# Optimization experiments

Measured on AMD Instinct MI355X. Metric: run time of the kernel, lower is better.

The kernel has to match this reference:

```python
import math
import jax, jax.numpy as jnp
import numpy as np
from jax import lax

B, H, W = 8, 96, 96
FC, R, P, KS, TOPK = 768, 12, 16, 13, 24
SUP_TH, SUP_MIX, OPEN_K, DIL, NMS = 0.28, 0.8, 3, 3, 3

# prototype anchor metadata (buffers, deterministic)
ORI = jnp.asarray(np.linspace(0.0, math.pi, P + 1)[:-1], jnp.float32)
_lenL = np.array([0.4, 0.7, 1.0, 1.25], np.float32)
_widL = np.array([0.12, 0.18, 0.24, 0.3], np.float32)
LEN = jnp.asarray(_lenL[np.arange(P) % 4])
WID = jnp.asarray(_widL[(np.arange(P) // 4) % 4])
_ax = np.linspace(-1.0, 1.0, KS).astype(np.float32)
_gy, _gx = np.meshgrid(_ax, _ax, indexing='ij')
GX, GY = jnp.asarray(_gx), jnp.asarray(_gy)


def conv2d(x, w, b, pad=0):
    y = lax.conv_general_dilated(x, w, (1, 1), [(pad, pad), (pad, pad)],
                                 dimension_numbers=('NCHW', 'OIHW', 'NCHW'))
    return y + b[None, :, None, None]


def maxpool(x, k):
    p = k // 2
    return lax.reduce_window(x, -jnp.inf, lax.max, (1, 1, k, k), (1, 1, 1, 1),
                             [(0, 0), (0, 0), (p, p), (p, p)])


def avgpool3(x):
    s = lax.reduce_window(x, 0.0, lax.add, (1, 1, 3, 3), (1, 1, 1, 1),
                          [(0, 0), (0, 0), (1, 1), (1, 1)])
    return s / 9.0  # torch count_include_pad=True


def normalize_map(t):
    mn = t.min(axis=(-2, -1), keepdims=True)
    mx = t.max(axis=(-2, -1), keepdims=True)
    return (t - mn) / jnp.maximum(mx - mn, 1e-6)


def binary_open(m, k):
    er = 1.0 - maxpool(1.0 - m, k)
    return jnp.clip(maxpool(er, k), 0.0, 1.0)


def support_mask_fn(carrier_hp, density):
    cs = normalize_map(avgpool3(jnp.abs(carrier_hp)))
    ds = normalize_map(density)
    ev = SUP_MIX * cs + (1.0 - SUP_MIX) * ds
    m = (ev >= SUP_TH).astype(carrier_hp.dtype)
    m = binary_open(m, OPEN_K)
    m = maxpool(m, DIL)
    return jnp.clip(m, 0.0, 1.0)


def setup_inputs() -> dict:
    key = jax.random.key(0)
    ks = jax.random.split(key, 16)
    d = {
        'features': jax.random.normal(ks[0], (B, FC, H, W), jnp.float32),
        'carrier_hp': jax.random.normal(ks[1], (B, 1, H, W), jnp.float32),
        'density': jax.random.uniform(ks[2], (B, 1, H, W), jnp.float32),
        # feature_project: 1x1 conv FC->R, 3x3 conv R->R
        'w1': jax.random.normal(ks[3], (R, FC, 1, 1), jnp.float32) * (1.0 / math.sqrt(FC)),
        'b1': jnp.zeros((R,), jnp.float32),
        'w2': jax.random.normal(ks[4], (R, R, 3, 3), jnp.float32) * (1.0 / math.sqrt(R * 9)),
        'b2': jnp.zeros((R,), jnp.float32),
        # post_mix: 1x1 conv (R+4)->R, 1x1 conv R->FC
        'w3': jax.random.normal(ks[5], (R, R + 4, 1, 1), jnp.float32) * (1.0 / math.sqrt(R + 4)),
        'b3': jnp.zeros((R,), jnp.float32),
        'w4': jax.random.normal(ks[6], (FC, R, 1, 1), jnp.float32) * (1.0 / math.sqrt(R)),
        'b4': jnp.zeros((FC,), jnp.float32),
        'proto': jax.random.normal(ks[7], (P, R), jnp.float32) * 0.02,
    }
    return d


def reference(features, carrier_hp, density, w1, b1, w2, b2, w3, b3, w4, b4, proto):
    gelu = lambda x: jax.nn.gelu(x, approximate=False)
    # 1) feature projection
    proj = gelu(conv2d(gelu(conv2d(features, w1, b1, 0)), w2, b2, 1))  # [B,R,H,W]
    # 2) occupancy + support
    occ = normalize_map(jnp.abs(proj).mean(axis=1, keepdims=True))      # [B,1,H,W]
    sup = support_mask_fn(carrier_hp, density)                          # [B,1,H,W]
    # 3) NMS + top-k anchors
    scores = occ * sup
    local_max = maxpool(scores, NMS)
    peak = ((scores >= local_max) & (scores > 0.05)).astype(scores.dtype)
    flat = (scores * peak).reshape(B, -1)
    vals, idx = lax.top_k(flat, TOPK)                                   # [B,K]
    anchor_map = jnp.zeros_like(flat).at[jnp.arange(B)[:, None], idx].set(vals)
    anchor_map = anchor_map.reshape(B, 1, H, W)
    ys, xs = idx // W, idx % W
    # 4) per-anchor prototype selection
    proj_flat = proj.reshape(B, R, H * W)
    feat_at = jnp.take_along_axis(proj_flat, jnp.broadcast_to(idx[:, None, :], (B, R, TOPK)), axis=2)  # [B,R,K]
    logits = jnp.einsum('brk,pr->bkp', feat_at, proto)
    pidx = jnp.argmax(logits, axis=-1)                                  # [B,K]
    ori, ln, wd = ORI[pidx], LEN[pidx], WID[pidx]
    # 5) oriented Gaussian footprints [B,K,KS,KS]
    c = jnp.cos(ori)[..., None, None]
    s = jnp.sin(ori)[..., None, None]
    xr = c * GX + s * GY
    yr = -s * GX + c * GY
    foot = jnp.exp(-(xr / ln[..., None, None]) ** 2 - (yr / wd[..., None, None]) ** 2)
    foot = foot * vals[..., None, None]
    emb = proto[pidx]                                                   # [B,K,R]
    contrib = emb[:, :, :, None, None] * foot[:, :, None]               # [B,K,R,KS,KS]
    # 6) scatter-stamp onto canvas
    off = jnp.arange(KS) - KS // 2
    yy = ys[:, :, None, None] + off[None, None, :, None]                # [B,K,KS,KS]
    xx = xs[:, :, None, None] + off[None, None, None, :]
    valid = ((yy >= 0) & (yy < H) & (xx >= 0) & (xx < W)).astype(contrib.dtype)
    yyc = jnp.clip(yy, 0, H - 1)
    xxc = jnp.clip(xx, 0, W - 1)

    def stamp(ctr, y2, x2, v):
        c0 = jnp.zeros((R, H, W), ctr.dtype)
        return c0.at[:, y2, x2].add(jnp.transpose(ctr, (1, 0, 2, 3)) * v[None])

    canvas = jax.vmap(stamp)(contrib, yyc, xxc, valid)                  # [B,R,H,W]
    # 7) support-lock + post mix
    canvas = canvas * sup
    extras = jnp.concatenate([occ, sup, anchor_map, normalize_map(density)], axis=1)
    mixed = conv2d(gelu(conv2d(jnp.concatenate([canvas, extras], axis=1), w3, b3, 0)), w4, b4, 0)
    return mixed
```

## Files before the change

kernel.cpp:

```cpp
#include <hip/hip_runtime.h>
#include <math.h>

#define Bn 8
#define Hh 96
#define Ww 96
#define NPIX 9216
#define FCn 768
#define Rr 12
#define Pp 16
#define KSn 13
#define TOPKn 24
#define CAPc 1536

__device__ __forceinline__ float gelu_f(float x) {
  return 0.5f * x * (1.0f + erff(x * 0.70710678118654752440f));
}

__global__ __launch_bounds__(256) void k_conv1_part(
    const float* __restrict__ feat, const float* __restrict__ w1,
    float* __restrict__ partial) {
  __shared__ float w1s[192 * 12];
  int s = blockIdx.x & 3;
  int pixblk = blockIdx.x >> 2;
  int c0 = s * 192;
  for (int i = threadIdx.x; i < 192 * 12; i += 256) {
    int c = i / 12, r = i % 12;
    w1s[i] = w1[r * FCn + c0 + c];
  }
  __syncthreads();
  int pix = pixblk * 256 + threadIdx.x;
  int b = pix / NPIX, hw = pix % NPIX;
  const float* fb = feat + (size_t)b * FCn * NPIX + (size_t)c0 * NPIX + hw;
  float acc[12];
#pragma unroll
  for (int r = 0; r < 12; r++) acc[r] = 0.f;
  for (int c = 0; c < 192; c += 8) {
    float f[8];
#pragma unroll
    for (int u = 0; u < 8; u++) f[u] = fb[(size_t)(c + u) * NPIX];
#pragma unroll
    for (int u = 0; u < 8; u++) {
#pragma unroll
      for (int r = 0; r < 12; r++)
        acc[r] = fmaf(f[u], w1s[(c + u) * 12 + r], acc[r]);
    }
  }
  float* outp = partial + (size_t)s * (Bn * Rr * NPIX) +
                (size_t)b * Rr * NPIX + hw;
#pragma unroll
  for (int r = 0; r < 12; r++) outp[(size_t)r * NPIX] = acc[r];
}

__global__ __launch_bounds__(256) void k_bias_gelu(
    const float* __restrict__ partial, const float* __restrict__ b1,
    float* __restrict__ t1) {
  int e = blockIdx.x * 256 + threadIdx.x;
  if (e >= Bn * Rr * NPIX) return;
  int r = (e / NPIX) % Rr;
  const size_t N = (size_t)Bn * Rr * NPIX;
  float v = ((partial[e] + partial[e + N]) + partial[e + 2 * N]) +
            partial[e + 3 * N] + b1[r];
  t1[e] = gelu_f(v);
}

__global__ __launch_bounds__(256) void k_conv2(
    const float* __restrict__ t1, const float* __restrict__ w2,
    const float* __restrict__ b2, const float* __restrict__ carrier,
    float* __restrict__ proj, float* __restrict__ occ_raw,
    float* __restrict__ cs_raw) {
  __shared__ float w2s[Rr * Rr * 9];
  __shared__ float b2s[Rr];
  for (int i = threadIdx.x; i < Rr * Rr * 9; i += 256) w2s[i] = w2[i];
  if (threadIdx.x < Rr) b2s[threadIdx.x] = b2[threadIdx.x];
  __syncthreads();
  int pix = blockIdx.x * 256 + threadIdx.x;
  int b = pix / NPIX, hw = pix % NPIX;
  int y = hw / Ww, x = hw % Ww;
  float acc[12];
#pragma unroll
  for (int r = 0; r < 12; r++) acc[r] = 0.f;
  const float* tb = t1 + (size_t)b * Rr * NPIX;
  for (int ri = 0; ri < Rr; ri++) {
    const float* tc = tb + (size_t)ri * NPIX;
#pragma unroll
    for (int ky = 0; ky < 3; ky++) {
      int yy = y + ky - 1;
      if (yy < 0 || yy >= Hh) continue;
#pragma unroll
      for (int kx = 0; kx < 3; kx++) {
        int xx = x + kx - 1;
        if (xx < 0 || xx >= Ww) continue;
        float v = tc[yy * Ww + xx];
#pragma unroll
        for (int ro = 0; ro < 12; ro++)
          acc[ro] = fmaf(v, w2s[((ro * Rr + ri) * 3 + ky) * 3 + kx], acc[ro]);
      }
    }
  }
  float asum = 0.f;
  float* pb = proj + (size_t)b * Rr * NPIX + hw;
#pragma unroll
  for (int ro = 0; ro < 12; ro++) {
    float g = gelu_f(acc[ro] + b2s[ro]);
    pb[(size_t)ro * NPIX] = g;
    asum += fabsf(g);
  }
  occ_raw[pix] = asum / 12.0f;

  const float* cb = carrier + (size_t)b * NPIX;
  float s9 = 0.f;
  for (int dy = -1; dy <= 1; dy++) {
    int yy = y + dy;
    if (yy < 0 || yy >= Hh) continue;
    for (int dx = -1; dx <= 1; dx++) {
      int xx = x + dx;
      if (xx < 0 || xx >= Ww) continue;
      s9 += fabsf(cb[yy * Ww + xx]);
    }
  }
  cs_raw[pix] = s9 / 9.0f;
}

__global__ __launch_bounds__(256) void k_minmax(
    const float* __restrict__ occ_raw, const float* __restrict__ cs_raw,
    const float* __restrict__ density, float* __restrict__ stats) {
  int a = blockIdx.x / Bn, b = blockIdx.x % Bn;
  const float* src = (a == 0) ? occ_raw : (a == 1) ? cs_raw : density;
  src += (size_t)b * NPIX;
  __shared__ float smn[256], smx[256];
  float mn = INFINITY, mx = -INFINITY;
  for (int p = threadIdx.x; p < NPIX; p += 256) {
    float v = src[p];
    mn = fminf(mn, v);
    mx = fmaxf(mx, v);
  }
  smn[threadIdx.x] = mn;
  smx[threadIdx.x] = mx;
  __syncthreads();
  for (int s = 128; s > 0; s >>= 1) {
    if (threadIdx.x < s) {
      smn[threadIdx.x] = fminf(smn[threadIdx.x], smn[threadIdx.x + s]);
      smx[threadIdx.x] = fmaxf(smx[threadIdx.x], smx[threadIdx.x + s]);
    }
    __syncthreads();
  }
  if (threadIdx.x == 0) {
    stats[(a * Bn + b) * 2 + 0] = smn[0];
    stats[(a * Bn + b) * 2 + 1] = smx[0];
  }
}

__global__ __launch_bounds__(1024) void k_support(
    const float* __restrict__ occ_raw, const float* __restrict__ cs_raw,
    const float* __restrict__ density, const float* __restrict__ stats,
    float* __restrict__ occ, float* __restrict__ ds, float* __restrict__ sup,
    float* __restrict__ scores) {
  __shared__ unsigned char mA[NPIX], mB[NPIX];
  int b = blockIdx.x;
  float omn = stats[(0 * Bn + b) * 2], omx = stats[(0 * Bn + b) * 2 + 1];
  float cmn = stats[(1 * Bn + b) * 2], cmx = stats[(1 * Bn + b) * 2 + 1];
  float dmn = stats[(2 * Bn + b) * 2], dmx = stats[(2 * Bn + b) * 2 + 1];
  float oiv = fmaxf(omx - omn, 1e-6f);
  float civ = fmaxf(cmx - cmn, 1e-6f);
  float div_ = fmaxf(dmx - dmn, 1e-6f);
  float occ9[9];
#pragma unroll
  for (int i = 0; i < 9; i++) {
    int p = threadIdx.x + i * 1024;
    float oc = (occ_raw[b * NPIX + p] - omn) / oiv;
    float cv = (cs_raw[b * NPIX + p] - cmn) / civ;
    float dv = (density[b * NPIX + p] - dmn) / div_;
    occ[b * NPIX + p] = oc;
    ds[b * NPIX + p] = dv;
    occ9[i] = oc;
    float ev = 0.8f * cv + 0.2f * dv;
    mA[p] = (ev >= 0.28f) ? 1 : 0;
  }
  __syncthreads();
#pragma unroll
  for (int i = 0; i < 9; i++) {
    int p = threadIdx.x + i * 1024;
    int y = p / Ww, x = p % Ww;
    unsigned char m = 1;
    for (int dy = -1; dy <= 1; dy++) {
      int yy = y + dy;
      if (yy < 0 || yy >= Hh) continue;
      for (int dx = -1; dx <= 1; dx++) {
        int xx = x + dx;
        if (xx < 0 || xx >= Ww) continue;
        m = (unsigned char)(m & mA[yy * Ww + xx]);
      }
    }
    mB[p] = m;
  }
  __syncthreads();
#pragma unroll
  for (int i = 0; i < 9; i++) {
    int p = threadIdx.x + i * 1024;
    int y = p / Ww, x = p % Ww;
    unsigned char m = 0;
    for (int dy = -1; dy <= 1; dy++) {
      int yy = y + dy;
      if (yy < 0 || yy >= Hh) continue;
      for (int dx = -1; dx <= 1; dx++) {
        int xx = x + dx;
        if (xx < 0 || xx >= Ww) continue;
        m = (unsigned char)(m | mB[yy * Ww + xx]);
      }
    }
    mA[p] = m;
  }
  __syncthreads();
#pragma unroll
  for (int i = 0; i < 9; i++) {
    int p = threadIdx.x + i * 1024;
    int y = p / Ww, x = p % Ww;
    unsigned char m = 0;
    for (int dy = -1; dy <= 1; dy++) {
      int yy = y + dy;
      if (yy < 0 || yy >= Hh) continue;
      for (int dx = -1; dx <= 1; dx++) {
        int xx = x + dx;
        if (xx < 0 || xx >= Ww) continue;
        m = (unsigned char)(m | mA[yy * Ww + xx]);
      }
    }
    float sv = (float)m;
    sup[b * NPIX + p] = sv;
    scores[b * NPIX + p] = occ9[i] * sv;
  }
}

__global__ __launch_bounds__(256) void k_topk(
    const float* __restrict__ scores, float* __restrict__ vals,
    int* __restrict__ idxs, float* __restrict__ anchor) {
  __shared__ float flat[NPIX];
  __shared__ float cval[CAPc];
  __shared__ int cidx[CAPc];
  __shared__ int cnt;
  __shared__ float rv[4];
  __shared__ int ri[4], rs[4];
  int b = blockIdx.x;
  const int tid = threadIdx.x;
  const int lane = tid & 63, wid = tid >> 6;
  const float* sc = scores + (size_t)b * NPIX;
#pragma unroll
  for (int i = 0; i < NPIX / 256; i++) flat[tid + i * 256] = sc[tid + i * 256];
  if (tid == 0) cnt = 0;
  __syncthreads();
  float pk[NPIX / 256];
#pragma unroll
  for (int i = 0; i < NPIX / 256; i++) {
    int p = tid + i * 256;
    int y = p / Ww, x = p % Ww;
    float s = flat[p];
    float lm = -INFINITY;
    for (int dy = -1; dy <= 1; dy++) {
      int yy = y + dy;
      if (yy < 0 || yy >= Hh) continue;
      for (int dx = -1; dx <= 1; dx++) {
        int xx = x + dx;
        if (xx < 0 || xx >= Ww) continue;
        lm = fmaxf(lm, flat[yy * Ww + xx]);
      }
    }
    pk[i] = (s >= lm && s > 0.05f) ? s : 0.0f;
  }
  __syncthreads();
#pragma unroll
  for (int i = 0; i < NPIX / 256; i++) {
    int p = tid + i * 256;
    flat[p] = pk[i];
    if (pk[i] > 0.f) {
      int slot = atomicAdd(&cnt, 1);
      if (slot < CAPc) {
        cval[slot] = pk[i];
        cidx[slot] = p;
      }
    }
  }
  __syncthreads();
  const int C = cnt;
  if (C <= CAPc) {
    for (int k = 0; k < TOPKn; k++) {
      float bv = -INFINITY;
      int bi = 0x7fffffff, bs = -1;
      for (int j = tid; j < C; j += 256) {
        float v = cval[j];
        int pi = cidx[j];
        if (v > bv || (v == bv && pi < bi)) {
          bv = v;
          bi = pi;
          bs = j;
        }
      }
      for (int off = 32; off > 0; off >>= 1) {
        float ov = __shfl_xor(bv, off);
        int oi = __shfl_xor(bi, off);
        int os = __shfl_xor(bs, off);
        if (ov > bv || (ov == bv && oi < bi)) {
          bv = ov;
          bi = oi;
          bs = os;
        }
      }
      if (lane == 0) {
        rv[wid] = bv;
        ri[wid] = bi;
        rs[wid] = bs;
      }
      __syncthreads();
      if (tid == 0) {
        float Bv = rv[0];
        int Bi = ri[0], Bs = rs[0];
        for (int w = 1; w < 4; w++) {
          if (rv[w] > Bv || (rv[w] == Bv && ri[w] < Bi)) {
            Bv = rv[w];
            Bi = ri[w];
            Bs = rs[w];
          }
        }
        if (Bv > 0.f) {
          vals[b * TOPKn + k] = Bv;
          idxs[b * TOPKn + k] = Bi;
          anchor[b * NPIX + Bi] = Bv;
          cval[Bs] = -INFINITY;
        } else {
          vals[b * TOPKn + k] = 0.f;
          idxs[b * TOPKn + k] = 0;
        }
      }
      __syncthreads();
    }
  } else {
    for (int k = 0; k < TOPKn; k++) {
      float bv = -INFINITY;
      int bi = 0x7fffffff;
      for (int p = tid; p < NPIX; p += 256) {
        float v = flat[p];
        if (v > bv || (v == bv && p < bi)) {
          bv = v;
          bi = p;
        }
      }
      for (int off = 32; off > 0; off >>= 1) {
        float ov = __shfl_xor(bv, off);
        int oi = __shfl_xor(bi, off);
        if (ov > bv || (ov == bv && oi < bi)) {
          bv = ov;
          bi = oi;
        }
      }
      if (lane == 0) {
        rv[wid] = bv;
        ri[wid] = bi;
      }
      __syncthreads();
      if (tid == 0) {
        float Bv = rv[0];
        int Bi = ri[0];
        for (int w = 1; w < 4; w++) {
          if (rv[w] > Bv || (rv[w] == Bv && ri[w] < Bi)) {
            Bv = rv[w];
            Bi = ri[w];
          }
        }
        if (Bv > 0.f) {
          vals[b * TOPKn + k] = Bv;
          idxs[b * TOPKn + k] = Bi;
          anchor[b * NPIX + Bi] = Bv;
          flat[Bi] = -INFINITY;
        } else {
          vals[b * TOPKn + k] = 0.f;
          idxs[b * TOPKn + k] = 0;
        }
      }
      __syncthreads();
    }
  }
}

__global__ __launch_bounds__(192) void k_stamp(
    const float* __restrict__ proj, const float* __restrict__ proto,
    const float* __restrict__ vals, const int* __restrict__ idxs,
    float* __restrict__ canvas) {
  int b = blockIdx.x / TOPKn, k = blockIdx.x % TOPKn;
  __shared__ float embs[12];
  __shared__ float prm[5];
  __shared__ int ppos[2];
  if (threadIdx.x == 0) {
    int id = idxs[b * TOPKn + k];
    float v = vals[b * TOPKn + k];
    float ft[12];
    for (int r = 0; r < 12; r++)
      ft[r] = proj[(size_t)(b * Rr + r) * NPIX + id];
    float bestL = -INFINITY;
    int bp = 0;
    for (int p = 0; p < Pp; p++) {
      float L = 0.f;
      for (int r = 0; r < 12; r++) L = fmaf(ft[r], proto[p * Rr + r], L);
      if (L > bestL) {
        bestL = L;
        bp = p;
      }
    }
    const float lenL[4] = {0.4f, 0.7f, 1.0f, 1.25f};
    const float widL[4] = {0.12f, 0.18f, 0.24f, 0.3f};
    float ori = (float)((M_PI / 16.0) * (double)bp);
    prm[0] = cosf(ori);
    prm[1] = sinf(ori);
    prm[2] = lenL[bp & 3];
    prm[3] = widL[(bp >> 2) & 3];
    prm[4] = v;
    ppos[0] = id / Ww;
    ppos[1] = id % Ww;
    for (int r = 0; r < 12; r++) embs[r] = proto[bp * Rr + r];
  }
  __syncthreads();
  float v = prm[4];
  if (v <= 0.f) return;
  int t = threadIdx.x;
  if (t >= KSn * KSn) return;
  int i = t / KSn, j = t % KSn;
  float gx = (float)(-1.0 + (double)j * (1.0 / 6.0));
  float gy = (float)(-1.0 + (double)i * (1.0 / 6.0));
  float c = prm[0], s = prm[1];
  float xr = c * gx + s * gy;
  float yr = -s * gx + c * gy;
  float tx = xr / prm[2], ty = yr / prm[3];
  float foot = expf(-(tx * tx) - (ty * ty)) * v;
  int yy = ppos[0] + i - KSn / 2;
  int xx = ppos[1] + j - KSn / 2;
  if (yy < 0 || yy >= Hh || xx < 0 || xx >= Ww) return;
  float* cp = canvas + (size_t)b * Rr * NPIX + yy * Ww + xx;
#pragma unroll
  for (int r = 0; r < 12; r++) atomicAdd(cp + (size_t)r * NPIX, embs[r] * foot);
}

__global__ __launch_bounds__(256) void k_post1(
    const float* __restrict__ canvas, const float* __restrict__ sup,
    const float* __restrict__ occ, const float* __restrict__ anchor,
    const float* __restrict__ ds, const float* __restrict__ w3,
    const float* __restrict__ b3, float* __restrict__ h) {
  __shared__ float w3s[12 * 16], b3s[12];
  for (int i = threadIdx.x; i < 192; i += 256) w3s[i] = w3[i];
  if (threadIdx.x < 12) b3s[threadIdx.x] = b3[threadIdx.x];
  __syncthreads();
  int pix = blockIdx.x * 256 + threadIdx.x;
  int b = pix / NPIX, hw = pix % NPIX;
  float in16[16];
  float sv = sup[pix];
#pragma unroll
  for (int r = 0; r < 12; r++)
    in16[r] = canvas[(size_t)(b * Rr + r) * NPIX + hw] * sv;
  in16[12] = occ[pix];
  in16[13] = sv;
  in16[14] = anchor[pix];
  in16[15] = ds[pix];
  float* hb = h + (size_t)b * Rr * NPIX + hw;
#pragma unroll
  for (int ro = 0; ro < 12; ro++) {
    float acc = 0.f;
#pragma unroll
    for (int ci = 0; ci < 16; ci++)
      acc = fmaf(in16[ci], w3s[ro * 16 + ci], acc);
    hb[(size_t)ro * NPIX] = gelu_f(acc + b3s[ro]);
  }
}

__global__ __launch_bounds__(256) void k_post2(
    const float* __restrict__ h, const float* __restrict__ w4,
    const float* __restrict__ b4, float* __restrict__ out) {
  __shared__ float w4s[16 * 12], b4s[16];
  int bx = blockIdx.x;
  int hwblk = bx % 36;
  int g = (bx / 36) % 48;
  int b = bx / (36 * 48);
  int oc0 = g * 16;
  for (int i = threadIdx.x; i < 192; i += 256) w4s[i] = w4[oc0 * 12 + i];
  if (threadIdx.x < 16) b4s[threadIdx.x] = b4[oc0 + threadIdx.x];
  __syncthreads();
  int hw = hwblk * 256 + threadIdx.x;
  float hreg[12];
  const float* hb = h + (size_t)b * Rr * NPIX + hw;
#pragma unroll
  for (int r = 0; r < 12; r++) hreg[r] = hb[(size_t)r * NPIX];
  float* ob = out + (size_t)(b * FCn + oc0) * NPIX + hw;
#pragma unroll
  for (int j = 0; j < 16; j++) {
    float acc = 0.f;
#pragma unroll
    for (int r = 0; r < 12; r++) acc = fmaf(hreg[r], w4s[j * 12 + r], acc);
    ob[(size_t)j * NPIX] = acc + b4s[j];
  }
}

extern "C" void kernel_launch(void* const* d_in, const int* in_sizes, int n_in,
                              void* d_out, int out_size, void* d_ws,
                              size_t ws_size, hipStream_t stream) {
  const float* features = (const float*)d_in[0];
  const float* carrier = (const float*)d_in[1];
  const float* density = (const float*)d_in[2];
  const float* w1 = (const float*)d_in[3];
  const float* b1 = (const float*)d_in[4];
  const float* w2 = (const float*)d_in[5];
  const float* b2 = (const float*)d_in[6];
  const float* w3 = (const float*)d_in[7];
  const float* b3 = (const float*)d_in[8];
  const float* w4 = (const float*)d_in[9];
  const float* b4 = (const float*)d_in[10];
  const float* proto = (const float*)d_in[11];
  float* out = (float*)d_out;
  float* ws = (float*)d_ws;

  const size_t NT = (size_t)Bn * Rr * NPIX;
  float* t1 = ws;
  float* partial = ws + NT;
  float* proj = partial;
  float* canvas = partial + NT;
  float* h = partial + 2 * NT;
  float* sm = ws + 5 * NT;
  float* occ_raw = sm;
  float* cs_raw = sm + (size_t)Bn * NPIX;
  float* occ = sm + 2 * (size_t)Bn * NPIX;
  float* ds = sm + 3 * (size_t)Bn * NPIX;
  float* sup = sm + 4 * (size_t)Bn * NPIX;
  float* scores = sm + 5 * (size_t)Bn * NPIX;
  float* anchor = sm + 6 * (size_t)Bn * NPIX;
  float* stats = sm + 7 * (size_t)Bn * NPIX;
  float* vals = stats + 64;
  int* idxs = (int*)(vals + Bn * TOPKn);

  k_conv1_part<<<288 * 4, 256, 0, stream>>>(features, w1, partial);
  k_bias_gelu<<<(int)((NT + 255) / 256), 256, 0, stream>>>(partial, b1, t1);
  hipMemsetAsync(canvas, 0, NT * sizeof(float), stream);
  hipMemsetAsync(anchor, 0, (size_t)Bn * NPIX * sizeof(float), stream);
  k_conv2<<<288, 256, 0, stream>>>(t1, w2, b2, carrier, proj, occ_raw, cs_raw);
  k_minmax<<<24, 256, 0, stream>>>(occ_raw, cs_raw, density, stats);
  k_support<<<Bn, 1024, 0, stream>>>(occ_raw, cs_raw, density, stats, occ, ds,
                                     sup, scores);
  k_topk<<<Bn, 256, 0, stream>>>(scores, vals, idxs, anchor);
  k_stamp<<<Bn * TOPKn, 192, 0, stream>>>(proj, proto, vals, idxs, canvas);
  k_post1<<<288, 256, 0, stream>>>(canvas, sup, occ, anchor, ds, w3, b3, h);
  k_post2<<<Bn * 48 * 36, 256, 0, stream>>>(h, w4, b4, out);
}
```

Before: 581.7 us.

## Vectorize conv1/post2 memory ops, fuse min-max stats and memsets into conv2

k_conv1_part now computes two pixels per thread with float2 loads. k_post2 computes four pixels per thread with float4 loads and stores, and k_bias_gelu works on float4. The separate k_minmax kernel and the two memsets are removed. conv2 now zeroes canvas and anchor, and reduces per-batch min/max with wave shuffles plus unsigned atomicMin/Max, with the stats initialised in k_bias_gelu. This cuts launches and raises memory-access width, but conv1 now runs half as many blocks. The unsigned-bit min/max trick is only correct for non-negative floats, which holds for these maps (abs-based values and uniform density).

```diff
diff --git a/kernel.cpp b/kernel.cpp
--- a/kernel.cpp
+++ b/kernel.cpp
@@ -28,52 +28,75 @@
     w1s[i] = w1[r * FCn + c0 + c];
   }
   __syncthreads();
-  int pix = pixblk * 256 + threadIdx.x;
-  int b = pix / NPIX, hw = pix % NPIX;
+  int px0 = pixblk * 512 + threadIdx.x * 2;
+  int b = px0 / NPIX, hw = px0 % NPIX;
   const float* fb = feat + (size_t)b * FCn * NPIX + (size_t)c0 * NPIX + hw;
-  float acc[12];
-#pragma unroll
-  for (int r = 0; r < 12; r++) acc[r] = 0.f;
-  for (int c = 0; c < 192; c += 8) {
-    float f[8];
-#pragma unroll
-    for (int u = 0; u < 8; u++) f[u] = fb[(size_t)(c + u) * NPIX];
-#pragma unroll
-    for (int u = 0; u < 8; u++) {
-#pragma unroll
-      for (int r = 0; r < 12; r++)
-        acc[r] = fmaf(f[u], w1s[(c + u) * 12 + r], acc[r]);
+  float acc0[12], acc1[12];
+#pragma unroll
+  for (int r = 0; r < 12; r++) { acc0[r] = 0.f; acc1[r] = 0.f; }
+  for (int c = 0; c < 192; c += 4) {
+    float2 f[4];
+#pragma unroll
+    for (int u = 0; u < 4; u++)
+      f[u] = *(const float2*)(fb + (size_t)(c + u) * NPIX);
+#pragma unroll
+    for (int u = 0; u < 4; u++) {
+#pragma unroll
+      for (int r = 0; r < 12; r++) {
+        float w = w1s[(c + u) * 12 + r];
+        acc0[r] = fmaf(f[u].x, w, acc0[r]);
+        acc1[r] = fmaf(f[u].y, w, acc1[r]);
+      }
     }
   }
   float* outp = partial + (size_t)s * (Bn * Rr * NPIX) +
                 (size_t)b * Rr * NPIX + hw;
 #pragma unroll
-  for (int r = 0; r < 12; r++) outp[(size_t)r * NPIX] = acc[r];
+  for (int r = 0; r < 12; r++)
+    *(float2*)(outp + (size_t)r * NPIX) = make_float2(acc0[r], acc1[r]);
 }
 
 __global__ __launch_bounds__(256) void k_bias_gelu(
     const float* __restrict__ partial, const float* __restrict__ b1,
-    float* __restrict__ t1) {
-  int e = blockIdx.x * 256 + threadIdx.x;
-  if (e >= Bn * Rr * NPIX) return;
-  int r = (e / NPIX) % Rr;
-  const size_t N = (size_t)Bn * Rr * NPIX;
-  float v = ((partial[e] + partial[e + N]) + partial[e + 2 * N]) +
-            partial[e + 3 * N] + b1[r];
-  t1[e] = gelu_f(v);
+    float* __restrict__ t1, unsigned int* __restrict__ statsu) {
+  int e4 = blockIdx.x * 256 + threadIdx.x;
+  const int Q = (Bn * Rr * NPIX) / 4;
+  const float4* pp = (const float4*)partial;
+  float4 a = pp[e4], b_ = pp[e4 + Q], c = pp[e4 + 2 * Q], d = pp[e4 + 3 * Q];
+  int r = (e4 / (NPIX / 4)) % Rr;
+  float bias = b1[r];
+  float4 v;
+  v.x = gelu_f(((a.x + b_.x) + c.x) + d.x + bias);
+  v.y = gelu_f(((a.y + b_.y) + c.y) + d.y + bias);
+  v.z = gelu_f(((a.z + b_.z) + c.z) + d.z + bias);
+  v.w = gelu_f(((a.w + b_.w) + c.w) + d.w + bias);
+  ((float4*)t1)[e4] = v;
+  if (e4 < 24) {
+    statsu[e4 * 2 + 0] = 0x7f800000u;
+    statsu[e4 * 2 + 1] = 0u;
+  }
 }
 
 __global__ __launch_bounds__(256) void k_conv2(
     const float* __restrict__ t1, const float* __restrict__ w2,
     const float* __restrict__ b2, const float* __restrict__ carrier,
-    float* __restrict__ proj, float* __restrict__ occ_raw,
-    float* __restrict__ cs_raw) {
+    const float* __restrict__ density, float* __restrict__ proj,
+    float* __restrict__ occ_raw, float* __restrict__ cs_raw,
+    unsigned int* __restrict__ statsu, float* __restrict__ canvas,
+    float* __restrict__ anchor) {
   __shared__ float w2s[Rr * Rr * 9];
   __shared__ float b2s[Rr];
   for (int i = threadIdx.x; i < Rr * Rr * 9; i += 256) w2s[i] = w2[i];
   if (threadIdx.x < Rr) b2s[threadIdx.x] = b2[threadIdx.x];
-  __syncthreads();
   int pix = blockIdx.x * 256 + threadIdx.x;
+  {
+    float4 z = make_float4(0.f, 0.f, 0.f, 0.f);
+    float4* c4 = (float4*)canvas;
+#pragma unroll
+    for (int q = 0; q < 3; q++) c4[(size_t)q * (Bn * NPIX) + pix] = z;
+    anchor[pix] = 0.f;
+  }
+  __syncthreads();
   int b = pix / NPIX, hw = pix % NPIX;
   int y = hw / Ww, x = hw % Ww;
   float acc[12];
@@ -105,7 +128,8 @@
     pb[(size_t)ro * NPIX] = g;
     asum += fabsf(g);
   }
-  occ_raw[pix] = asum / 12.0f;
+  float occv = asum / 12.0f;
+  occ_raw[pix] = occv;
 
   const float* cb = carrier + (size_t)b * NPIX;
   float s9 = 0.f;
@@ -118,35 +142,27 @@
       s9 += fabsf(cb[yy * Ww + xx]);
     }
   }
-  cs_raw[pix] = s9 / 9.0f;
-}
-
-__global__ __launch_bounds__(256) void k_minmax(
-    const float* __restrict__ occ_raw, const float* __restrict__ cs_raw,
-    const float* __restrict__ density, float* __restrict__ stats) {
-  int a = blockIdx.x / Bn, b = blockIdx.x % Bn;
-  const float* src = (a == 0) ? occ_raw : (a == 1) ? cs_raw : density;
-  src += (size_t)b * NPIX;
-  __shared__ float smn[256], smx[256];
-  float mn = INFINITY, mx = -INFINITY;
-  for (int p = threadIdx.x; p < NPIX; p += 256) {
-    float v = src[p];
-    mn = fminf(mn, v);
-    mx = fmaxf(mx, v);
-  }
-  smn[threadIdx.x] = mn;
-  smx[threadIdx.x] = mx;
-  __syncthreads();
-  for (int s = 128; s > 0; s >>= 1) {
-    if (threadIdx.x < s) {
-      smn[threadIdx.x] = fminf(smn[threadIdx.x], smn[threadIdx.x + s]);
-      smx[threadIdx.x] = fmaxf(smx[threadIdx.x], smx[threadIdx.x + s]);
-    }
-    __syncthreads();
-  }
-  if (threadIdx.x == 0) {
-    stats[(a * Bn + b) * 2 + 0] = smn[0];
-    stats[(a * Bn + b) * 2 + 1] = smx[0];
+  float csv = s9 / 9.0f;
+  cs_raw[pix] = csv;
+  float dv = density[pix];
+
+  float mn0 = occv, mx0 = occv, mn1 = csv, mx1 = csv, mn2 = dv, mx2 = dv;
+#pragma unroll
+  for (int off = 32; off > 0; off >>= 1) {
+    mn0 = fminf(mn0, __shfl_xor(mn0, off));
+    mx0 = fmaxf(mx0, __shfl_xor(mx0, off));
+    mn1 = fminf(mn1, __shfl_xor(mn1, off));
+    mx1 = fmaxf(mx1, __shfl_xor(mx1, off));
+    mn2 = fminf(mn2, __shfl_xor(mn2, off));
+    mx2 = fmaxf(mx2, __shfl_xor(mx2, off));
+  }
+  if ((threadIdx.x & 63) == 0) {
+    atomicMin(&statsu[(0 * Bn + b) * 2 + 0], __float_as_uint(mn0));
+    atomicMax(&statsu[(0 * Bn + b) * 2 + 1], __float_as_uint(mx0));
+    atomicMin(&statsu[(1 * Bn + b) * 2 + 0], __float_as_uint(mn1));
+    atomicMax(&statsu[(1 * Bn + b) * 2 + 1], __float_as_uint(mx1));
+    atomicMin(&statsu[(2 * Bn + b) * 2 + 0], __float_as_uint(mn2));
+    atomicMax(&statsu[(2 * Bn + b) * 2 + 1], __float_as_uint(mx2));
   }
 }
 
@@ -473,25 +489,34 @@
     const float* __restrict__ b4, float* __restrict__ out) {
   __shared__ float w4s[16 * 12], b4s[16];
   int bx = blockIdx.x;
-  int hwblk = bx % 36;
-  int g = (bx / 36) % 48;
-  int b = bx / (36 * 48);
+  int hwblk = bx % 9;
+  int g = (bx / 9) % 48;
+  int b = bx / (9 * 48);
   int oc0 = g * 16;
   for (int i = threadIdx.x; i < 192; i += 256) w4s[i] = w4[oc0 * 12 + i];
   if (threadIdx.x < 16) b4s[threadIdx.x] = b4[oc0 + threadIdx.x];
   __syncthreads();
-  int hw = hwblk * 256 + threadIdx.x;
-  float hreg[12];
+  int hw = hwblk * 1024 + threadIdx.x * 4;
   const float* hb = h + (size_t)b * Rr * NPIX + hw;
-#pragma unroll
-  for (int r = 0; r < 12; r++) hreg[r] = hb[(size_t)r * NPIX];
+  float4 hreg[12];
+#pragma unroll
+  for (int r = 0; r < 12; r++)
+    hreg[r] = *(const float4*)(hb + (size_t)r * NPIX);
   float* ob = out + (size_t)(b * FCn + oc0) * NPIX + hw;
 #pragma unroll
   for (int j = 0; j < 16; j++) {
-    float acc = 0.f;
-#pragma unroll
-    for (int r = 0; r < 12; r++) acc = fmaf(hreg[r], w4s[j * 12 + r], acc);
-    ob[(size_t)j * NPIX] = acc + b4s[j];
+    float ax = 0.f, ay = 0.f, az = 0.f, aw = 0.f;
+#pragma unroll
+    for (int r = 0; r < 12; r++) {
+      float w = w4s[j * 12 + r];
+      ax = fmaf(hreg[r].x, w, ax);
+      ay = fmaf(hreg[r].y, w, ay);
+      az = fmaf(hreg[r].z, w, az);
+      aw = fmaf(hreg[r].w, w, aw);
+    }
+    float bb = b4s[j];
+    *(float4*)(ob + (size_t)j * NPIX) =
+        make_float4(ax + bb, ay + bb, az + bb, aw + bb);
   }
 }
 
@@ -528,19 +553,18 @@
   float* scores = sm + 5 * (size_t)Bn * NPIX;
   float* anchor = sm + 6 * (size_t)Bn * NPIX;
   float* stats = sm + 7 * (size_t)Bn * NPIX;
+  unsigned int* statsu = (unsigned int*)stats;
   float* vals = stats + 64;
   int* idxs = (int*)(vals + Bn * TOPKn);
 
-  k_conv1_part<<<288 * 4, 256, 0, stream>>>(features, w1, partial);
-  k_bias_gelu<<<(int)((NT + 255) / 256), 256, 0, stream>>>(partial, b1, t1);
-  hipMemsetAsync(canvas, 0, NT * sizeof(float), stream);
-  hipMemsetAsync(anchor, 0, (size_t)Bn * NPIX * sizeof(float), stream);
-  k_conv2<<<288, 256, 0, stream>>>(t1, w2, b2, carrier, proj, occ_raw, cs_raw);
-  k_minmax<<<24, 256, 0, stream>>>(occ_raw, cs_raw, density, stats);
+  k_conv1_part<<<144 * 4, 256, 0, stream>>>(features, w1, partial);
+  k_bias_gelu<<<(int)(NT / 4 / 256), 256, 0, stream>>>(partial, b1, t1, statsu);
+  k_conv2<<<288, 256, 0, stream>>>(t1, w2, b2, carrier, density, proj, occ_raw,
+                                   cs_raw, statsu, canvas, anchor);
   k_support<<<Bn, 1024, 0, stream>>>(occ_raw, cs_raw, density, stats, occ, ds,
                                      sup, scores);
   k_topk<<<Bn, 256, 0, stream>>>(scores, vals, idxs, anchor);
   k_stamp<<<Bn * TOPKn, 192, 0, stream>>>(proj, proto, vals, idxs, canvas);
   k_post1<<<288, 256, 0, stream>>>(canvas, sup, occ, anchor, ds, w3, b3, h);
-  k_post2<<<Bn * 48 * 36, 256, 0, stream>>>(h, w4, b4, out);
-}
+  k_post2<<<Bn * 48 * 9, 256, 0, stream>>>(h, w4, b4, out);
+}
```

Result: faster. 562.4 us (-3.3%).
